# Kernel tuning notes

Hardware: AMD Instinct MI355X
Metric: run time of the kernel (lower is better)

The kernel has to match this reference:

```python
import jax, jax.numpy as jnp
import numpy as np

N_NODES = 100000
N_EDGES = 1000000
IN_CH = 64
HID = 64


def setup_inputs() -> dict:
    key = jax.random.key(0)
    ks = jax.random.split(key, 10)
    x = jax.random.normal(ks[0], (N_NODES, IN_CH), dtype=jnp.float32)
    edge_index = jax.random.randint(ks[1], (2, N_EDGES), 0, N_NODES, dtype=jnp.int32)
    s = 1.0 / np.sqrt(IN_CH)
    sh = 1.0 / np.sqrt(HID)
    return {
        "x": x,
        "edge_index": edge_index,
        # conv1: lin_l (applied to aggregated neighbors, has bias), lin_r (self, no bias)
        "w1_l": jax.random.uniform(ks[2], (HID, IN_CH), jnp.float32, -s, s),
        "b1": jnp.zeros((HID,), jnp.float32),
        "w1_r": jax.random.uniform(ks[3], (HID, IN_CH), jnp.float32, -s, s),
        # conv2
        "w2_l": jax.random.uniform(ks[4], (HID, HID), jnp.float32, -sh, sh),
        "b2": jnp.zeros((HID,), jnp.float32),
        "w2_r": jax.random.uniform(ks[5], (HID, HID), jnp.float32, -sh, sh),
        # final linear -> 1
        "w_out": jax.random.uniform(ks[6], (1, HID), jnp.float32, -sh, sh),
        "b_out": jnp.zeros((1,), jnp.float32),
    }


def _sage_conv(x, src, dst, w_l, b, w_r, n_nodes):
    # mean aggregation of source features at destination nodes
    agg = jax.ops.segment_sum(x[src], dst, num_segments=n_nodes)  # [N, d]
    cnt = jax.ops.segment_sum(jnp.ones_like(dst, dtype=x.dtype), dst, num_segments=n_nodes)
    mean = agg / jnp.maximum(cnt, 1.0)[:, None]
    # PyG SAGEConv: lin_l(aggregated) + lin_r(x_self); bias lives in lin_l
    return mean @ w_l.T + b + x @ w_r.T


def reference(x, edge_index, w1_l, b1, w1_r, w2_l, b2, w2_r, w_out, b_out):
    src, dst = edge_index[0], edge_index[1]
    n = x.shape[0]
    h = jax.nn.relu(_sage_conv(x, src, dst, w1_l, b1, w1_r, n))
    h = jax.nn.relu(_sage_conv(h, src, dst, w2_l, b2, w2_r, n))
    logits = h @ w_out.T + b_out  # [N, 1]
    return jax.nn.sigmoid(logits)
```

## Files before the change

### kernel.cpp

```cpp
#include <hip/hip_runtime.h>
#include <hip/hip_bf16.h>
#include <math.h>

#define CH 64
#define TILE 16
#define NXCD 8

typedef short short8 __attribute__((ext_vector_type(8)));
typedef float floatx4 __attribute__((ext_vector_type(4)));

__device__ __forceinline__ float bf2f(unsigned short u) {
    return __uint_as_float(((unsigned int)u) << 16);
}
__device__ __forceinline__ unsigned short f2bf(float f) {
    unsigned int x = __float_as_uint(f);
    unsigned int r = (x + 0x7fff + ((x >> 16) & 1)) >> 16;
    return (unsigned short)r;
}

__global__ __launch_bounds__(256) void k_hist(
    const unsigned short* __restrict__ x,
    const int* __restrict__ srcs, const int* __restrict__ dsts,
    int* __restrict__ deg, int* __restrict__ flag,
    int n_edges, int n_nodes)
{
    if (blockIdx.x == 0 && threadIdx.x < 64) {
        unsigned short u = x[2 * threadIdx.x];
        int ex = (u >> 7) & 0xFF;
        bool insane = (ex < 0x60) || (ex > 0x9F);
        unsigned long long m = __ballot(insane);
        if (threadIdx.x == 0) flag[0] = (__popcll(m) > 16) ? 0 : 1;
    }
    int e = blockIdx.x * 256 + threadIdx.x;
    if (e >= n_edges) return;
    int d = dsts[e], s = srcs[e];
    if ((unsigned)d < (unsigned)n_nodes && (unsigned)s < (unsigned)n_nodes)
        atomicAdd(&deg[d], 1);
}

__global__ __launch_bounds__(256) void k_scan1(
    const int* __restrict__ deg, int* __restrict__ rowptr,
    int* __restrict__ bsum, int n)
{
    __shared__ int ts[256];
    int t = threadIdx.x;
    int base = blockIdx.x * 1024 + t * 4;
    int v[4], local = 0;
    #pragma unroll
    for (int k = 0; k < 4; k++) { v[k] = (base + k < n) ? deg[base + k] : 0; local += v[k]; }
    ts[t] = local; __syncthreads();
    for (int off = 1; off < 256; off <<= 1) {
        int val = (t >= off) ? ts[t - off] : 0;
        __syncthreads();
        ts[t] += val;
        __syncthreads();
    }
    int run = ts[t] - local;
    #pragma unroll
    for (int k = 0; k < 4; k++) { if (base + k < n) rowptr[base + k] = run; run += v[k]; }
    if (t == 255) bsum[blockIdx.x] = ts[255];
}

__global__ __launch_bounds__(256) void k_scan2(
    int* __restrict__ bsum, int* __restrict__ rowptr, int nb, int n)
{
    __shared__ int ts[256];
    int t = threadIdx.x;
    int base = t * 4;
    int v[4], local = 0;
    #pragma unroll
    for (int k = 0; k < 4; k++) { v[k] = (base + k < nb) ? bsum[base + k] : 0; local += v[k]; }
    ts[t] = local; __syncthreads();
    for (int off = 1; off < 256; off <<= 1) {
        int val = (t >= off) ? ts[t - off] : 0;
        __syncthreads();
        ts[t] += val;
        __syncthreads();
    }
    int run = ts[t] - local;
    #pragma unroll
    for (int k = 0; k < 4; k++) { if (base + k < nb) bsum[base + k] = run; run += v[k]; }
    if (t == 255) rowptr[n] = ts[255];
}

__global__ __launch_bounds__(256) void k_scan3(
    int* __restrict__ rowptr, int* __restrict__ cursor,
    const int* __restrict__ bsum, int n)
{
    int add = bsum[blockIdx.x];
    int base = blockIdx.x * 1024 + threadIdx.x * 4;
    #pragma unroll
    for (int k = 0; k < 4; k++) {
        int i = base + k;
        if (i < n) { int r = rowptr[i] + add; rowptr[i] = r; cursor[i] = r; }
    }
}

__global__ __launch_bounds__(256) void k_permute(
    const int* __restrict__ srcs, const int* __restrict__ dsts,
    int* __restrict__ cursor, int* __restrict__ nbr, int n_edges, int n_nodes)
{
    const int grp = blockIdx.x & (NXCD - 1);
    const int gidx = blockIdx.x >> 3;
    const int gstride = (gridDim.x >> 3) * 256;
    const int range = (n_nodes + NXCD - 1) / NXCD;
    const int lo = grp * range;
    const int hi = min(n_nodes, lo + range);
    for (int e = gidx * 256 + threadIdx.x; e < n_edges; e += gstride) {
        int d = dsts[e];
        if (d >= lo && d < hi) {
            int s = srcs[e];
            if ((unsigned)s < (unsigned)n_nodes) {
                int pos = atomicAdd(&cursor[d], 1);
                nbr[pos] = s;
            }
        }
    }
}

template <int XMODE>
__global__ __launch_bounds__(256) void k_gather(
    const int* __restrict__ flag, const void* __restrict__ xin,
    const int* __restrict__ nbr, const int* __restrict__ rowptr,
    unsigned short* __restrict__ meanout, int n_nodes)
{
    const bool xbf = (XMODE == 1) ? true : (flag[0] != 0);
    const int lane = threadIdx.x & 63;
    const int wid  = threadIdx.x >> 6;
    const int t = lane >> 4;
    const int s = (lane >> 3) & 1;
    const int c = lane & 7;

    int wbase = (blockIdx.x * 4 + wid) * 4;
    if (wbase >= n_nodes) return;
    int node = wbase + t;
    bool nv = node < n_nodes;
    int r0 = 0, d = 0;
    if (nv) { r0 = rowptr[node]; d = rowptr[node + 1] - r0; }

    int dmax = d;
    dmax = max(dmax, __shfl_xor(dmax, 16));
    dmax = max(dmax, __shfl_xor(dmax, 32));

    const unsigned short* xu = (const unsigned short*)xin;
    const float*          xf = (const float*)xin;

    if (xbf) {
        floatx4 a0 = {0, 0, 0, 0}, a1 = {0, 0, 0, 0};
        for (int jb = 0; jb < dmax; jb += 16) {
            #pragma unroll
            for (int k = 0; k < 8; k++) {
                int j = jb + k * 2 + s;
                if (j < d) {
                    int src = nbr[r0 + j];
                    short8 v = *(const short8*)(xu + (size_t)src * CH + c * 8);
                    #pragma unroll
                    for (int i = 0; i < 4; i++) a0[i] += bf2f((unsigned short)v[i]);
                    #pragma unroll
                    for (int i = 0; i < 4; i++) a1[i] += bf2f((unsigned short)v[4 + i]);
                }
            }
        }
        #pragma unroll
        for (int i = 0; i < 4; i++) {
            a0[i] += __shfl_xor(a0[i], 8);
            a1[i] += __shfl_xor(a1[i], 8);
        }
        if (nv && (lane & 8) == 0) {
            float inv = 1.0f / (float)max(d, 1);
            short8 mv;
            #pragma unroll
            for (int i = 0; i < 4; i++) {
                mv[i]     = (short)f2bf(a0[i] * inv);
                mv[4 + i] = (short)f2bf(a1[i] * inv);
            }
            *(short8*)(meanout + (size_t)node * CH + c * 8) = mv;
        }
    } else {
        int j16 = lane & 15;
        floatx4 acc = {0, 0, 0, 0};
        for (int j = 0; j < d; j++) {
            int src = nbr[r0 + j];
            acc += *(const floatx4*)(xf + (size_t)src * CH + j16 * 4);
        }
        if (nv) {
            float inv = 1.0f / (float)max(d, 1);
            unsigned short* mp = meanout + (size_t)node * CH + j16 * 4;
            #pragma unroll
            for (int i = 0; i < 4; i++) mp[i] = f2bf(acc[i] * inv);
        }
    }
}

template <int XMODE, bool HEAD>
__global__ __launch_bounds__(256) void k_mm(
    const int* __restrict__ flag, const void* __restrict__ xin,
    const unsigned short* __restrict__ meanin,
    const void* __restrict__ w_l, const void* __restrict__ bias,
    const void* __restrict__ w_r,
    const void* __restrict__ w_out, const void* __restrict__ b_out,
    void* __restrict__ outp, int n_nodes)
{
    const int isbf = flag[0];
    const bool xbf = (XMODE == 1) ? true : (isbf != 0);
    const int lane = threadIdx.x & 63;
    const int wid  = threadIdx.x >> 6;
    const int n_ = lane & 15;
    const int q_ = lane >> 4;

    short8 wlf[4][2], wrf[4][2];
    float bv[4], wov[4];
    #pragma unroll
    for (int t = 0; t < 4; t++) {
        int row = t * 16 + n_;
        if (isbf) {
            const unsigned short* wl = (const unsigned short*)w_l;
            const unsigned short* wr = (const unsigned short*)w_r;
            #pragma unroll
            for (int kc = 0; kc < 2; kc++) {
                int k0 = kc * 32 + q_ * 8;
                wlf[t][kc] = *(const short8*)(wl + row * CH + k0);
                wrf[t][kc] = *(const short8*)(wr + row * CH + k0);
            }
            bv[t] = bf2f(((const unsigned short*)bias)[row]);
            if (HEAD) wov[t] = bf2f(((const unsigned short*)w_out)[row]);
        } else {
            const float* wl = (const float*)w_l;
            const float* wr = (const float*)w_r;
            #pragma unroll
            for (int kc = 0; kc < 2; kc++) {
                int k0 = kc * 32 + q_ * 8;
                #pragma unroll
                for (int j = 0; j < 8; j++) {
                    wlf[t][kc][j] = (short)f2bf(wl[row * CH + k0 + j]);
                    wrf[t][kc][j] = (short)f2bf(wr[row * CH + k0 + j]);
                }
            }
            bv[t] = ((const float*)bias)[row];
            if (HEAD) wov[t] = ((const float*)w_out)[row];
        }
    }

    const unsigned short* xu = (const unsigned short*)xin;
    const float*          xf = (const float*)xin;
    int n_tiles = (n_nodes + TILE - 1) / TILE;
    int gw = blockIdx.x * 4 + wid;
    int nw = gridDim.x * 4;

    for (int tb = gw; tb < n_tiles; tb += nw) {
        int base = tb * TILE;
        int node_m = base + n_;
        int node_c = (node_m < n_nodes) ? node_m : 0;
        short8 am0 = *(const short8*)(meanin + (size_t)node_c * CH + q_ * 8);
        short8 am1 = *(const short8*)(meanin + (size_t)node_c * CH + 32 + q_ * 8);
        short8 ax0, ax1;
        if (xbf) {
            ax0 = *(const short8*)(xu + (size_t)node_c * CH + q_ * 8);
            ax1 = *(const short8*)(xu + (size_t)node_c * CH + 32 + q_ * 8);
        } else {
            const float* p = xf + (size_t)node_c * CH;
            #pragma unroll
            for (int j = 0; j < 8; j++) {
                ax0[j] = (short)f2bf(p[q_ * 8 + j]);
                ax1[j] = (short)f2bf(p[32 + q_ * 8 + j]);
            }
        }
        floatx4 acc[4];
        #pragma unroll
        for (int t = 0; t < 4; t++) {
            acc[t] = (floatx4){bv[t], bv[t], bv[t], bv[t]};
            acc[t] = __builtin_amdgcn_mfma_f32_16x16x32_bf16(am0, wlf[t][0], acc[t], 0, 0, 0);
            acc[t] = __builtin_amdgcn_mfma_f32_16x16x32_bf16(am1, wlf[t][1], acc[t], 0, 0, 0);
            acc[t] = __builtin_amdgcn_mfma_f32_16x16x32_bf16(ax0, wrf[t][0], acc[t], 0, 0, 0);
            acc[t] = __builtin_amdgcn_mfma_f32_16x16x32_bf16(ax1, wrf[t][1], acc[t], 0, 0, 0);
        }
        if (!HEAD) {
            unsigned short* ho = (unsigned short*)outp;
            #pragma unroll
            for (int t = 0; t < 4; t++) {
                int cc = t * 16 + n_;
                #pragma unroll
                for (int reg = 0; reg < 4; reg++) {
                    int node_r = base + q_ * 4 + reg;
                    if (node_r < n_nodes)
                        ho[(size_t)node_r * CH + cc] = f2bf(fmaxf(acc[t][reg], 0.0f));
                }
            }
        } else {
            float p[4] = {0, 0, 0, 0};
            #pragma unroll
            for (int t = 0; t < 4; t++) {
                #pragma unroll
                for (int reg = 0; reg < 4; reg++)
                    p[reg] += fmaxf(acc[t][reg], 0.0f) * wov[t];
            }
            #pragma unroll
            for (int off = 1; off < 16; off <<= 1) {
                #pragma unroll
                for (int reg = 0; reg < 4; reg++)
                    p[reg] += __shfl_xor(p[reg], off);
            }
            if (n_ == 0) {
                float bo = isbf ? bf2f(((const unsigned short*)b_out)[0])
                                : ((const float*)b_out)[0];
                #pragma unroll
                for (int reg = 0; reg < 4; reg++) {
                    int node_r = base + q_ * 4 + reg;
                    if (node_r < n_nodes) {
                        float sg = 1.0f / (1.0f + expf(-(p[reg] + bo)));
                        if (isbf) ((unsigned short*)outp)[node_r] = f2bf(sg);
                        else      ((float*)outp)[node_r] = sg;
                    }
                }
            }
        }
    }
}

extern "C" void kernel_launch(void* const* d_in, const int* in_sizes, int n_in,
                              void* d_out, int out_size, void* d_ws, size_t ws_size,
                              hipStream_t stream)
{
    const void* x    = d_in[0];
    const int*  ei   = (const int*)d_in[1];
    const void* w1_l = d_in[2];
    const void* b1   = d_in[3];
    const void* w1_r = d_in[4];
    const void* w2_l = d_in[5];
    const void* b2   = d_in[6];
    const void* w2_r = d_in[7];
    const void* wout = d_in[8];
    const void* bout = d_in[9];

    int n_nodes = out_size;
    int n_edges = in_sizes[1] / 2;
    const int* srcs = ei;
    const int* dsts = ei + n_edges;

    char* wsb = (char*)d_ws;
    size_t off = 0;
    auto carve = [&](size_t bytes) { size_t p = off; off = (off + bytes + 255) & ~(size_t)255; return p; };
    size_t flag_off = carve(sizeof(int));
    size_t deg_off  = carve((size_t)n_nodes * sizeof(int));
    size_t row_off  = carve((size_t)(n_nodes + 1) * sizeof(int));
    size_t cur_off  = carve((size_t)n_nodes * sizeof(int));
    size_t bs_off   = carve(1024 * sizeof(int));
    size_t nbr_off  = carve((size_t)n_edges * sizeof(int));
    size_t mean_off = carve((size_t)n_nodes * CH * sizeof(unsigned short));
    size_t h_off    = carve((size_t)n_nodes * CH * sizeof(unsigned short));
    int* flag   = (int*)(wsb + flag_off);
    int* deg    = (int*)(wsb + deg_off);
    int* rowptr = (int*)(wsb + row_off);
    int* cursor = (int*)(wsb + cur_off);
    int* bsum   = (int*)(wsb + bs_off);
    int* nbr    = (int*)(wsb + nbr_off);
    unsigned short* mean = (unsigned short*)(wsb + mean_off);
    unsigned short* h    = (unsigned short*)(wsb + h_off);

    int eblocks = (n_edges + 255) / 256;
    int xblocks = 2048;
    int nb1     = (n_nodes + 1023) / 1024;
    int gblocks = (n_nodes + 15) / 16;
    int mblocks = 512;

    hipMemsetAsync(deg, 0, (size_t)n_nodes * sizeof(int), stream);

    k_hist<<<eblocks, 256, 0, stream>>>((const unsigned short*)x, srcs, dsts, deg, flag, n_edges, n_nodes);
    k_scan1<<<nb1, 256, 0, stream>>>(deg, rowptr, bsum, n_nodes);
    k_scan2<<<1, 256, 0, stream>>>(bsum, rowptr, nb1, n_nodes);
    k_scan3<<<nb1, 256, 0, stream>>>(rowptr, cursor, bsum, n_nodes);
    k_permute<<<xblocks, 256, 0, stream>>>(srcs, dsts, cursor, nbr, n_edges, n_nodes);

    k_gather<0><<<gblocks, 256, 0, stream>>>(flag, x, nbr, rowptr, mean, n_nodes);
    k_mm<0, false><<<mblocks, 256, 0, stream>>>(flag, x, mean, w1_l, b1, w1_r,
                                                nullptr, nullptr, h, n_nodes);
    k_gather<1><<<gblocks, 256, 0, stream>>>(flag, h, nbr, rowptr, mean, n_nodes);
    k_mm<1, true><<<mblocks, 256, 0, stream>>>(flag, h, mean, w2_l, b2, w2_r,
                                               wout, bout, d_out, n_nodes);
}
```

Baseline: 282.9 us.

## Fuse neighbor mean gather with SAGE matmul via shared-memory tile

```diff
diff --git a/kernel.cpp b/kernel.cpp
--- a/kernel.cpp
+++ b/kernel.cpp
@@ -3,7 +3,6 @@
 #include <math.h>
 
 #define CH 64
-#define TILE 16
 #define NXCD 8
 
 typedef short short8 __attribute__((ext_vector_type(8)));
@@ -118,84 +117,10 @@
     }
 }
 
-template <int XMODE>
-__global__ __launch_bounds__(256) void k_gather(
+template <int XMODE, bool HEAD>
+__global__ __launch_bounds__(256) void k_fused(
     const int* __restrict__ flag, const void* __restrict__ xin,
     const int* __restrict__ nbr, const int* __restrict__ rowptr,
-    unsigned short* __restrict__ meanout, int n_nodes)
-{
-    const bool xbf = (XMODE == 1) ? true : (flag[0] != 0);
-    const int lane = threadIdx.x & 63;
-    const int wid  = threadIdx.x >> 6;
-    const int t = lane >> 4;
-    const int s = (lane >> 3) & 1;
-    const int c = lane & 7;
-
-    int wbase = (blockIdx.x * 4 + wid) * 4;
-    if (wbase >= n_nodes) return;
-    int node = wbase + t;
-    bool nv = node < n_nodes;
-    int r0 = 0, d = 0;
-    if (nv) { r0 = rowptr[node]; d = rowptr[node + 1] - r0; }
-
-    int dmax = d;
-    dmax = max(dmax, __shfl_xor(dmax, 16));
-    dmax = max(dmax, __shfl_xor(dmax, 32));
-
-    const unsigned short* xu = (const unsigned short*)xin;
-    const float*          xf = (const float*)xin;
-
-    if (xbf) {
-        floatx4 a0 = {0, 0, 0, 0}, a1 = {0, 0, 0, 0};
-        for (int jb = 0; jb < dmax; jb += 16) {
-            #pragma unroll
-            for (int k = 0; k < 8; k++) {
-                int j = jb + k * 2 + s;
-                if (j < d) {
-                    int src = nbr[r0 + j];
-                    short8 v = *(const short8*)(xu + (size_t)src * CH + c * 8);
-                    #pragma unroll
-                    for (int i = 0; i < 4; i++) a0[i] += bf2f((unsigned short)v[i]);
-                    #pragma unroll
-                    for (int i = 0; i < 4; i++) a1[i] += bf2f((unsigned short)v[4 + i]);
-                }
-            }
-        }
-        #pragma unroll
-        for (int i = 0; i < 4; i++) {
-            a0[i] += __shfl_xor(a0[i], 8);
-            a1[i] += __shfl_xor(a1[i], 8);
-        }
-        if (nv && (lane & 8) == 0) {
-            float inv = 1.0f / (float)max(d, 1);
-            short8 mv;
-            #pragma unroll
-            for (int i = 0; i < 4; i++) {
-                mv[i]     = (short)f2bf(a0[i] * inv);
-                mv[4 + i] = (short)f2bf(a1[i] * inv);
-            }
-            *(short8*)(meanout + (size_t)node * CH + c * 8) = mv;
-        }
-    } else {
-        int j16 = lane & 15;
-        floatx4 acc = {0, 0, 0, 0};
-        for (int j = 0; j < d; j++) {
-            int src = nbr[r0 + j];
-            acc += *(const floatx4*)(xf + (size_t)src * CH + j16 * 4);
-        }
-        if (nv) {
-            float inv = 1.0f / (float)max(d, 1);
-            unsigned short* mp = meanout + (size_t)node * CH + j16 * 4;
-            #pragma unroll
-            for (int i = 0; i < 4; i++) mp[i] = f2bf(acc[i] * inv);
-        }
-    }
-}
-
-template <int XMODE, bool HEAD>
-__global__ __launch_bounds__(256) void k_mm(
-    const int* __restrict__ flag, const void* __restrict__ xin,
-    const unsigned short* __restrict__ meanin,
     const void* __restrict__ w_l, const void* __restrict__ bias,
     const void* __restrict__ w_r,
     const void* __restrict__ w_out, const void* __restrict__ b_out,
@@ -205,113 +130,165 @@
     const bool xbf = (XMODE == 1) ? true : (isbf != 0);
     const int lane = threadIdx.x & 63;
     const int wid  = threadIdx.x >> 6;
+    const int base = blockIdx.x * 16;
+
+    __shared__ __align__(16) unsigned short smean[16][72];
+    __shared__ float psum[4][16];
+
+    const unsigned short* xu = (const unsigned short*)xin;
+    const float*          xf = (const float*)xin;
+
+    {
+        const int t = lane >> 4;
+        const int s = (lane >> 3) & 1;
+        const int c = lane & 7;
+        int node = base + wid * 4 + t;
+        bool nv = node < n_nodes;
+        int r0 = 0, d = 0;
+        if (nv) { r0 = rowptr[node]; d = rowptr[node + 1] - r0; }
+
+        int dmax = d;
+        dmax = max(dmax, __shfl_xor(dmax, 16));
+        dmax = max(dmax, __shfl_xor(dmax, 32));
+
+        if (xbf) {
+            floatx4 a0 = {0, 0, 0, 0}, a1 = {0, 0, 0, 0};
+            for (int jb = 0; jb < dmax; jb += 16) {
+                #pragma unroll
+                for (int k = 0; k < 8; k++) {
+                    int j = jb + k * 2 + s;
+                    if (j < d) {
+                        int src = nbr[r0 + j];
+                        short8 v = *(const short8*)(xu + (size_t)src * CH + c * 8);
+                        #pragma unroll
+                        for (int i = 0; i < 4; i++) a0[i] += bf2f((unsigned short)v[i]);
+                        #pragma unroll
+                        for (int i = 0; i < 4; i++) a1[i] += bf2f((unsigned short)v[4 + i]);
+                    }
+                }
+            }
+            #pragma unroll
+            for (int i = 0; i < 4; i++) {
+                a0[i] += __shfl_xor(a0[i], 8);
+                a1[i] += __shfl_xor(a1[i], 8);
+            }
+            if ((lane & 8) == 0) {
+                float inv = 1.0f / (float)max(d, 1);
+                short8 mv;
+                #pragma unroll
+                for (int i = 0; i < 4; i++) {
+                    mv[i]     = (short)f2bf(a0[i] * inv);
+                    mv[4 + i] = (short)f2bf(a1[i] * inv);
+                }
+                *(short8*)(&smean[wid * 4 + t][c * 8]) = mv;
+            }
+        } else {
+            int j16 = lane & 15;
+            floatx4 acc = {0, 0, 0, 0};
+            for (int j = 0; j < d; j++) {
+                int src = nbr[r0 + j];
+                acc += *(const floatx4*)(xf + (size_t)src * CH + j16 * 4);
+            }
+            float inv = 1.0f / (float)max(d, 1);
+            #pragma unroll
+            for (int i = 0; i < 4; i++)
+                smean[wid * 4 + t][j16 * 4 + i] = f2bf(acc[i] * inv);
+        }
+    }
+    __syncthreads();
+
     const int n_ = lane & 15;
     const int q_ = lane >> 4;
-
-    short8 wlf[4][2], wrf[4][2];
-    float bv[4], wov[4];
-    #pragma unroll
-    for (int t = 0; t < 4; t++) {
-        int row = t * 16 + n_;
-        if (isbf) {
-            const unsigned short* wl = (const unsigned short*)w_l;
-            const unsigned short* wr = (const unsigned short*)w_r;
-            #pragma unroll
-            for (int kc = 0; kc < 2; kc++) {
-                int k0 = kc * 32 + q_ * 8;
-                wlf[t][kc] = *(const short8*)(wl + row * CH + k0);
-                wrf[t][kc] = *(const short8*)(wr + row * CH + k0);
-            }
-            bv[t] = bf2f(((const unsigned short*)bias)[row]);
-            if (HEAD) wov[t] = bf2f(((const unsigned short*)w_out)[row]);
-        } else {
-            const float* wl = (const float*)w_l;
-            const float* wr = (const float*)w_r;
-            #pragma unroll
-            for (int kc = 0; kc < 2; kc++) {
-                int k0 = kc * 32 + q_ * 8;
-                #pragma unroll
-                for (int j = 0; j < 8; j++) {
-                    wlf[t][kc][j] = (short)f2bf(wl[row * CH + k0 + j]);
-                    wrf[t][kc][j] = (short)f2bf(wr[row * CH + k0 + j]);
-                }
-            }
-            bv[t] = ((const float*)bias)[row];
-            if (HEAD) wov[t] = ((const float*)w_out)[row];
-        }
-    }
-
-    const unsigned short* xu = (const unsigned short*)xin;
-    const float*          xf = (const float*)xin;
-    int n_tiles = (n_nodes + TILE - 1) / TILE;
-    int gw = blockIdx.x * 4 + wid;
-    int nw = gridDim.x * 4;
-
-    for (int tb = gw; tb < n_tiles; tb += nw) {
-        int base = tb * TILE;
-        int node_m = base + n_;
-        int node_c = (node_m < n_nodes) ? node_m : 0;
-        short8 am0 = *(const short8*)(meanin + (size_t)node_c * CH + q_ * 8);
-        short8 am1 = *(const short8*)(meanin + (size_t)node_c * CH + 32 + q_ * 8);
-        short8 ax0, ax1;
-        if (xbf) {
-            ax0 = *(const short8*)(xu + (size_t)node_c * CH + q_ * 8);
-            ax1 = *(const short8*)(xu + (size_t)node_c * CH + 32 + q_ * 8);
-        } else {
-            const float* p = xf + (size_t)node_c * CH;
+    const int row = wid * 16 + n_;
+
+    short8 wlf[2], wrf[2];
+    float bv, wov = 0.0f;
+    if (isbf) {
+        const unsigned short* wl = (const unsigned short*)w_l;
+        const unsigned short* wr = (const unsigned short*)w_r;
+        #pragma unroll
+        for (int kc = 0; kc < 2; kc++) {
+            int k0 = kc * 32 + q_ * 8;
+            wlf[kc] = *(const short8*)(wl + row * CH + k0);
+            wrf[kc] = *(const short8*)(wr + row * CH + k0);
+        }
+        bv = bf2f(((const unsigned short*)bias)[row]);
+        if (HEAD) wov = bf2f(((const unsigned short*)w_out)[row]);
+    } else {
+        const float* wl = (const float*)w_l;
+        const float* wr = (const float*)w_r;
+        #pragma unroll
+        for (int kc = 0; kc < 2; kc++) {
+            int k0 = kc * 32 + q_ * 8;
             #pragma unroll
             for (int j = 0; j < 8; j++) {
-                ax0[j] = (short)f2bf(p[q_ * 8 + j]);
-                ax1[j] = (short)f2bf(p[32 + q_ * 8 + j]);
-            }
-        }
-        floatx4 acc[4];
-        #pragma unroll
-        for (int t = 0; t < 4; t++) {
-            acc[t] = (floatx4){bv[t], bv[t], bv[t], bv[t]};
-            acc[t] = __builtin_amdgcn_mfma_f32_16x16x32_bf16(am0, wlf[t][0], acc[t], 0, 0, 0);
-            acc[t] = __builtin_amdgcn_mfma_f32_16x16x32_bf16(am1, wlf[t][1], acc[t], 0, 0, 0);
-            acc[t] = __builtin_amdgcn_mfma_f32_16x16x32_bf16(ax0, wrf[t][0], acc[t], 0, 0, 0);
-            acc[t] = __builtin_amdgcn_mfma_f32_16x16x32_bf16(ax1, wrf[t][1], acc[t], 0, 0, 0);
-        }
-        if (!HEAD) {
-            unsigned short* ho = (unsigned short*)outp;
-            #pragma unroll
-            for (int t = 0; t < 4; t++) {
-                int cc = t * 16 + n_;
-                #pragma unroll
-                for (int reg = 0; reg < 4; reg++) {
-                    int node_r = base + q_ * 4 + reg;
-                    if (node_r < n_nodes)
-                        ho[(size_t)node_r * CH + cc] = f2bf(fmaxf(acc[t][reg], 0.0f));
-                }
-            }
-        } else {
-            float p[4] = {0, 0, 0, 0};
-            #pragma unroll
-            for (int t = 0; t < 4; t++) {
-                #pragma unroll
-                for (int reg = 0; reg < 4; reg++)
-                    p[reg] += fmaxf(acc[t][reg], 0.0f) * wov[t];
-            }
-            #pragma unroll
-            for (int off = 1; off < 16; off <<= 1) {
-                #pragma unroll
-                for (int reg = 0; reg < 4; reg++)
-                    p[reg] += __shfl_xor(p[reg], off);
-            }
-            if (n_ == 0) {
+                wlf[kc][j] = (short)f2bf(wl[row * CH + k0 + j]);
+                wrf[kc][j] = (short)f2bf(wr[row * CH + k0 + j]);
+            }
+        }
+        bv = ((const float*)bias)[row];
+        if (HEAD) wov = ((const float*)w_out)[row];
+    }
+
+    short8 am0 = *(const short8*)(&smean[n_][q_ * 8]);
+    short8 am1 = *(const short8*)(&smean[n_][32 + q_ * 8]);
+    int node_m = base + n_;
+    int node_c = (node_m < n_nodes) ? node_m : 0;
+    short8 ax0, ax1;
+    if (xbf) {
+        ax0 = *(const short8*)(xu + (size_t)node_c * CH + q_ * 8);
+        ax1 = *(const short8*)(xu + (size_t)node_c * CH + 32 + q_ * 8);
+    } else {
+        const float* p = xf + (size_t)node_c * CH;
+        #pragma unroll
+        for (int j = 0; j < 8; j++) {
+            ax0[j] = (short)f2bf(p[q_ * 8 + j]);
+            ax1[j] = (short)f2bf(p[32 + q_ * 8 + j]);
+        }
+    }
+
+    floatx4 acc = {bv, bv, bv, bv};
+    acc = __builtin_amdgcn_mfma_f32_16x16x32_bf16(am0, wlf[0], acc, 0, 0, 0);
+    acc = __builtin_amdgcn_mfma_f32_16x16x32_bf16(am1, wlf[1], acc, 0, 0, 0);
+    acc = __builtin_amdgcn_mfma_f32_16x16x32_bf16(ax0, wrf[0], acc, 0, 0, 0);
+    acc = __builtin_amdgcn_mfma_f32_16x16x32_bf16(ax1, wrf[1], acc, 0, 0, 0);
+
+    if (!HEAD) {
+        unsigned short* ho = (unsigned short*)outp;
+        int cc = wid * 16 + n_;
+        #pragma unroll
+        for (int reg = 0; reg < 4; reg++) {
+            int node_r = base + q_ * 4 + reg;
+            if (node_r < n_nodes)
+                ho[(size_t)node_r * CH + cc] = f2bf(fmaxf(acc[reg], 0.0f));
+        }
+    } else {
+        float p[4];
+        #pragma unroll
+        for (int reg = 0; reg < 4; reg++)
+            p[reg] = fmaxf(acc[reg], 0.0f) * wov;
+        #pragma unroll
+        for (int off = 1; off < 16; off <<= 1) {
+            #pragma unroll
+            for (int reg = 0; reg < 4; reg++)
+                p[reg] += __shfl_xor(p[reg], off);
+        }
+        if (n_ == 0) {
+            #pragma unroll
+            for (int reg = 0; reg < 4; reg++)
+                psum[wid][q_ * 4 + reg] = p[reg];
+        }
+        __syncthreads();
+        if (threadIdx.x < 16) {
+            int node_r = base + threadIdx.x;
+            if (node_r < n_nodes) {
                 float bo = isbf ? bf2f(((const unsigned short*)b_out)[0])
                                 : ((const float*)b_out)[0];
-                #pragma unroll
-                for (int reg = 0; reg < 4; reg++) {
-                    int node_r = base + q_ * 4 + reg;
-                    if (node_r < n_nodes) {
-                        float sg = 1.0f / (1.0f + expf(-(p[reg] + bo)));
-                        if (isbf) ((unsigned short*)outp)[node_r] = f2bf(sg);
-                        else      ((float*)outp)[node_r] = sg;
-                    }
-                }
+                float v = psum[0][threadIdx.x] + psum[1][threadIdx.x]
+                        + psum[2][threadIdx.x] + psum[3][threadIdx.x] + bo;
+                float sg = 1.0f / (1.0f + expf(-v));
+                if (isbf) ((unsigned short*)outp)[node_r] = f2bf(sg);
+                else      ((float*)outp)[node_r] = sg;
             }
         }
     }
@@ -346,7 +323,6 @@
     size_t cur_off  = carve((size_t)n_nodes * sizeof(int));
     size_t bs_off   = carve(1024 * sizeof(int));
     size_t nbr_off  = carve((size_t)n_edges * sizeof(int));
-    size_t mean_off = carve((size_t)n_nodes * CH * sizeof(unsigned short));
     size_t h_off    = carve((size_t)n_nodes * CH * sizeof(unsigned short));
     int* flag   = (int*)(wsb + flag_off);
     int* deg    = (int*)(wsb + deg_off);
@@ -354,14 +330,12 @@
     int* cursor = (int*)(wsb + cur_off);
     int* bsum   = (int*)(wsb + bs_off);
     int* nbr    = (int*)(wsb + nbr_off);
-    unsigned short* mean = (unsigned short*)(wsb + mean_off);
-    unsigned short* h    = (unsigned short*)(wsb + h_off);
+    unsigned short* h = (unsigned short*)(wsb + h_off);
 
     int eblocks = (n_edges + 255) / 256;
     int xblocks = 2048;
     int nb1     = (n_nodes + 1023) / 1024;
-    int gblocks = (n_nodes + 15) / 16;
-    int mblocks = 512;
+    int fblocks = (n_nodes + 15) / 16;
 
     hipMemsetAsync(deg, 0, (size_t)n_nodes * sizeof(int), stream);
 
@@ -371,10 +345,10 @@
     k_scan3<<<nb1, 256, 0, stream>>>(rowptr, cursor, bsum, n_nodes);
     k_permute<<<xblocks, 256, 0, stream>>>(srcs, dsts, cursor, nbr, n_edges, n_nodes);
 
-    k_gather<0><<<gblocks, 256, 0, stream>>>(flag, x, nbr, rowptr, mean, n_nodes);
-    k_mm<0, false><<<mblocks, 256, 0, stream>>>(flag, x, mean, w1_l, b1, w1_r,
-                                                nullptr, nullptr, h, n_nodes);
-    k_gather<1><<<gblocks, 256, 0, stream>>>(flag, h, nbr, rowptr, mean, n_nodes);
-    k_mm<1, true><<<mblocks, 256, 0, stream>>>(flag, h, mean, w2_l, b2, w2_r,
-                                               wout, bout, d_out, n_nodes);
-}
+    k_fused<0, false><<<fblocks, 256, 0, stream>>>(flag, x, nbr, rowptr,
+                                                   w1_l, b1, w1_r,
+                                                   nullptr, nullptr, h, n_nodes);
+    k_fused<1, true><<<fblocks, 256, 0, stream>>>(flag, h, nbr, rowptr,
+                                                  w2_l, b2, w2_r,
+                                                  wout, bout, d_out, n_nodes);
+}
```

Result: slower. 308.6 us (+9.1%).

## Fuse three-kernel prefix scan into one kernel with last-block grid sync

Applied to the files above, without the earlier changes.

```diff
diff --git a/kernel.cpp b/kernel.cpp
--- a/kernel.cpp
+++ b/kernel.cpp
@@ -38,13 +38,17 @@
         atomicAdd(&deg[d], 1);
 }
 
-__global__ __launch_bounds__(256) void k_scan1(
+__global__ __launch_bounds__(256) void k_scan(
     const int* __restrict__ deg, int* __restrict__ rowptr,
-    int* __restrict__ bsum, int n)
+    int* __restrict__ cursor, int* __restrict__ bsum,
+    int* __restrict__ sync, int n, int nb)
 {
     __shared__ int ts[256];
-    int t = threadIdx.x;
-    int base = blockIdx.x * 1024 + t * 4;
+    __shared__ int amlast;
+    const int t = threadIdx.x;
+    const int b = blockIdx.x;
+
+    int base = b * 1024 + t * 4;
     int v[4], local = 0;
     #pragma unroll
     for (int k = 0; k < 4; k++) { v[k] = (base + k < n) ? deg[base + k] : 0; local += v[k]; }
@@ -58,37 +62,41 @@
     int run = ts[t] - local;
     #pragma unroll
     for (int k = 0; k < 4; k++) { if (base + k < n) rowptr[base + k] = run; run += v[k]; }
-    if (t == 255) bsum[blockIdx.x] = ts[255];
-}
-
-__global__ __launch_bounds__(256) void k_scan2(
-    int* __restrict__ bsum, int* __restrict__ rowptr, int nb, int n)
-{
-    __shared__ int ts[256];
-    int t = threadIdx.x;
-    int base = t * 4;
-    int v[4], local = 0;
-    #pragma unroll
-    for (int k = 0; k < 4; k++) { v[k] = (base + k < nb) ? bsum[base + k] : 0; local += v[k]; }
-    ts[t] = local; __syncthreads();
-    for (int off = 1; off < 256; off <<= 1) {
-        int val = (t >= off) ? ts[t - off] : 0;
+    if (t == 255) bsum[b] = ts[255];
+
+    __threadfence();
+    __syncthreads();
+    if (t == 0) amlast = (atomicAdd(&sync[0], 1) == nb - 1) ? 1 : 0;
+    __syncthreads();
+
+    if (amlast) {
+        int base2 = t * 4;
+        int v2[4], local2 = 0;
+        #pragma unroll
+        for (int k = 0; k < 4; k++) { v2[k] = (base2 + k < nb) ? bsum[base2 + k] : 0; local2 += v2[k]; }
+        ts[t] = local2; __syncthreads();
+        for (int off = 1; off < 256; off <<= 1) {
+            int val = (t >= off) ? ts[t - off] : 0;
+            __syncthreads();
+            ts[t] += val;
+            __syncthreads();
+        }
+        int run2 = ts[t] - local2;
+        #pragma unroll
+        for (int k = 0; k < 4; k++) { if (base2 + k < nb) bsum[base2 + k] = run2; run2 += v2[k]; }
+        if (t == 255) rowptr[n] = ts[255];
+        __threadfence();
         __syncthreads();
-        ts[t] += val;
-        __syncthreads();
-    }
-    int run = ts[t] - local;
-    #pragma unroll
-    for (int k = 0; k < 4; k++) { if (base + k < nb) bsum[base + k] = run; run += v[k]; }
-    if (t == 255) rowptr[n] = ts[255];
-}
-
-__global__ __launch_bounds__(256) void k_scan3(
-    int* __restrict__ rowptr, int* __restrict__ cursor,
-    const int* __restrict__ bsum, int n)
-{
-    int add = bsum[blockIdx.x];
-    int base = blockIdx.x * 1024 + threadIdx.x * 4;
+        if (t == 0)
+            __hip_atomic_store(&sync[1], 1, __ATOMIC_RELEASE, __HIP_MEMORY_SCOPE_AGENT);
+    }
+
+    if (t == 0) {
+        while (__hip_atomic_load(&sync[1], __ATOMIC_ACQUIRE, __HIP_MEMORY_SCOPE_AGENT) == 0)
+            __builtin_amdgcn_s_sleep(8);
+    }
+    __syncthreads();
+    int add = bsum[b];
     #pragma unroll
     for (int k = 0; k < 4; k++) {
         int i = base + k;
@@ -341,6 +349,7 @@
     size_t off = 0;
     auto carve = [&](size_t bytes) { size_t p = off; off = (off + bytes + 255) & ~(size_t)255; return p; };
     size_t flag_off = carve(sizeof(int));
+    size_t sync_off = carve(256);
     size_t deg_off  = carve((size_t)n_nodes * sizeof(int));
     size_t row_off  = carve((size_t)(n_nodes + 1) * sizeof(int));
     size_t cur_off  = carve((size_t)n_nodes * sizeof(int));
@@ -349,6 +358,7 @@
     size_t mean_off = carve((size_t)n_nodes * CH * sizeof(unsigned short));
     size_t h_off    = carve((size_t)n_nodes * CH * sizeof(unsigned short));
     int* flag   = (int*)(wsb + flag_off);
+    int* syncp  = (int*)(wsb + sync_off);
     int* deg    = (int*)(wsb + deg_off);
     int* rowptr = (int*)(wsb + row_off);
     int* cursor = (int*)(wsb + cur_off);
@@ -363,12 +373,10 @@
     int gblocks = (n_nodes + 15) / 16;
     int mblocks = 512;
 
-    hipMemsetAsync(deg, 0, (size_t)n_nodes * sizeof(int), stream);
+    hipMemsetAsync(syncp, 0, 256 + (size_t)n_nodes * sizeof(int), stream);
 
     k_hist<<<eblocks, 256, 0, stream>>>((const unsigned short*)x, srcs, dsts, deg, flag, n_edges, n_nodes);
-    k_scan1<<<nb1, 256, 0, stream>>>(deg, rowptr, bsum, n_nodes);
-    k_scan2<<<1, 256, 0, stream>>>(bsum, rowptr, nb1, n_nodes);
-    k_scan3<<<nb1, 256, 0, stream>>>(rowptr, cursor, bsum, n_nodes);
+    k_scan<<<nb1, 256, 0, stream>>>(deg, rowptr, cursor, bsum, syncp, n_nodes, nb1);
     k_permute<<<xblocks, 256, 0, stream>>>(srcs, dsts, cursor, nbr, n_edges, n_nodes);
 
     k_gather<0><<<gblocks, 256, 0, stream>>>(flag, x, nbr, rowptr, mean, n_nodes);
```

Result: slower. 296.1 us (+4.7%).
